# Kernel tuning notes

Measured on AMD Instinct MI355X. Metric: run time of the kernel, lower is better.

Reference implementation:

```python
import jax, jax.numpy as jnp
import numpy as np

BATCH = 32768
NJETS = 10
NCOMBOS = 22
FF = 200
NSEL = 6
EPS = 1e-5
METRIC = jnp.array([1.0, -1.0, -1.0, -1.0], dtype=jnp.float32)  # (E,px,py,pz) Minkowski


def _cola(v, w_combo):
    # v: [b, n, 4]; w_combo: [c, n] -> [b, n+c, 4] (identity rows + learned combos)
    combos = jnp.einsum('cj,bjv->bcv', w_combo, v)
    return jnp.concatenate([v, combos], axis=1)


def _lola(v, w_e, w_d):
    # v: [b, n, 4] -> [b, n, 5] features: m2, pT, E, w_e.E, w_d.d2
    m2 = jnp.einsum('biv,v,biv->bi', v, METRIC, v)           # invariant mass^2
    pt = jnp.sqrt(v[..., 1] ** 2 + v[..., 2] ** 2)           # transverse momentum
    E = v[..., 0]
    we = jnp.einsum('ij,bj->bi', w_e, E)
    # pairwise Minkowski distances via gram trick (avoids [b,n,n,4] tensor)
    gram = jnp.einsum('biv,v,bjv->bij', v, METRIC, v)        # [b, n, n]
    d2 = m2[:, :, None] + m2[:, None, :] - 2.0 * gram
    wd = jnp.einsum('ij,bij->bi', w_d, d2)
    return jnp.stack([m2, pt, E, we, wd], axis=-1)


def _batchnorm(x, gamma, beta):
    # torch BatchNorm1d in train mode: per-feature batch mean / biased var
    mu = jnp.mean(x, axis=0)
    var = jnp.mean((x - mu) ** 2, axis=0)
    return (x - mu) * jax.lax.rsqrt(var + EPS) * gamma + beta


def _head(v, cola_w, w_e, w_d, bn_g, bn_b, w1, b1, w2, b2):
    x = _cola(v, cola_w)
    f = _lola(x, w_e, w_d).reshape(x.shape[0], -1)  # [b, ntotal*5]
    f = _batchnorm(f, bn_g, bn_b)
    h = jax.nn.relu(f @ w1.T + b1)
    return h @ w2.T + b2


def setup_inputs() -> dict:
    key = jax.random.key(0)
    ks = jax.random.split(key, 20)
    n_isr = NJETS + NCOMBOS   # 32
    n_dec = NSEL + NCOMBOS    # 28
    f_isr, f_dec = n_isr * 5, n_dec * 5
    rn = lambda k, s, sc=0.1: jax.random.normal(k, s, jnp.float32) * sc
    return {
        'vectors': jax.random.normal(ks[0], (BATCH, NJETS, 4), jnp.float32),
        'isr_cola_w': rn(ks[1], (NCOMBOS, NJETS)),
        'isr_we': rn(ks[2], (n_isr, n_isr)),
        'isr_wd': rn(ks[3], (n_isr, n_isr)),
        'isr_bn_g': jnp.ones((f_isr,), jnp.float32),
        'isr_bn_b': jnp.zeros((f_isr,), jnp.float32),
        'isr_w1': rn(ks[4], (FF, f_isr)),
        'isr_b1': jnp.zeros((FF,), jnp.float32),
        'isr_w2': rn(ks[5], (NJETS, FF)),
        'isr_b2': jnp.zeros((NJETS,), jnp.float32),
        'dec_cola_w': rn(ks[6], (NCOMBOS, NSEL)),
        'dec_we': rn(ks[7], (n_dec, n_dec)),
        'dec_wd': rn(ks[8], (n_dec, n_dec)),
        'dec_bn_g': jnp.ones((f_dec,), jnp.float32),
        'dec_bn_b': jnp.zeros((f_dec,), jnp.float32),
        'dec_w1': rn(ks[9], (FF, f_dec)),
        'dec_b1': jnp.zeros((FF,), jnp.float32),
        'dec_w2': rn(ks[10], (11, FF)),
        'dec_b2': jnp.zeros((11,), jnp.float32),
    }


def reference(vectors, isr_cola_w, isr_we, isr_wd, isr_bn_g, isr_bn_b,
              isr_w1, isr_b1, isr_w2, isr_b2,
              dec_cola_w, dec_we, dec_wd, dec_bn_g, dec_bn_b,
              dec_w1, dec_b1, dec_w2, dec_b2):
    out_isr = _head(vectors, isr_cola_w, isr_we, isr_wd, isr_bn_g, isr_bn_b,
                    isr_w1, isr_b1, isr_w2, isr_b2)  # [b, njets]
    # iterative argmin+delete of (njets-6) jets == keep top-6 scores, original order
    scores = jax.lax.stop_gradient(out_isr)  # torch code detaches isrtag
    _, idx = jax.lax.top_k(scores, NSEL)
    idx = jnp.sort(idx, axis=1)  # np.delete preserves original ordering
    selected = jnp.take_along_axis(vectors, idx[:, :, None], axis=1)  # [b, 6, 4]
    out_dec = _head(selected, dec_cola_w, dec_we, dec_wd, dec_bn_g, dec_bn_b,
                    dec_w1, dec_b1, dec_w2, dec_b2)  # [b, 11]
    return jnp.concatenate([out_isr, out_dec], axis=1)  # [b, njets+11]
```

## Files before the change

kernel.cpp:

```cpp
#include <hip/hip_runtime.h>


#define BATCH 32768
#define NJ 10
#define FFDIM 200
#define OUTSTRIDE 21
#define NFEATBLK 4096

typedef float v2f __attribute__((ext_vector_type(2)));

template<int NIN, int NP>
__global__ __launch_bounds__(256) void feat_kernel(
    const float* __restrict__ vin,
    const float* __restrict__ cola,
    const float* __restrict__ we,
    const float* __restrict__ wd,
    float* __restrict__ fout,
    float* __restrict__ psum,
    float* __restrict__ psq)
{
    constexpr int NC = 22;
    constexpr int F  = NP * 5;
    constexpr int RB = 8;
    constexpr int SW = NP + 1;
    constexpr int SF = F + 8;
    __shared__ float s_cola[NC * NIN];
    __shared__ float s_we[NP * SW];
    __shared__ float s_wd[NP * SW];
    __shared__ float4 s_x[RB][NP];
    __shared__ float s_m2[RB][NP];
    __shared__ float s_f[RB * SF];

    const int tid = threadIdx.x;
    const int blk = blockIdx.x;

    for (int k = tid; k < NC * NIN; k += 256) s_cola[k] = cola[k];
    for (int k = tid; k < NP * NP; k += 256) {
        const int i2 = k / NP, j2 = k - i2 * NP;
        s_we[i2 * SW + j2] = we[k];
        s_wd[i2 * SW + j2] = wd[k];
    }
    for (int k = tid; k < RB * NIN * 4; k += 256)
        ((float*)&s_x[0][0])[(k / (NIN * 4)) * NP * 4 + (k % (NIN * 4))] =
            vin[(size_t)blk * RB * NIN * 4 + k];
    __syncthreads();

    const int r = tid >> 5;
    const int i = tid & 31;

    if (i >= NIN && i < NP) {
        const int c = i - NIN;
        float4 x = make_float4(0.f, 0.f, 0.f, 0.f);
        #pragma unroll
        for (int j = 0; j < NIN; j++) {
            const float w = s_cola[c * NIN + j];
            const float4 xj = s_x[r][j];
            x.x += w * xj.x; x.y += w * xj.y; x.z += w * xj.z; x.w += w * xj.w;
        }
        s_x[r][i] = x;
    }
    __syncthreads();

    float m2 = 0.f, pt = 0.f;
    float4 xi = make_float4(0.f, 0.f, 0.f, 0.f);
    if (i < NP) {
        xi = s_x[r][i];
        m2 = xi.x * xi.x - xi.y * xi.y - xi.z * xi.z - xi.w * xi.w;
        pt = sqrtf(xi.y * xi.y + xi.z * xi.z);
        s_m2[r][i] = m2;
    }
    __syncthreads();
    if (i < NP) {
        float wesum = 0.f, wdsum = 0.f;
        for (int j = 0; j < NP; j++) {
            const float4 xj = s_x[r][j];
            wesum += s_we[i * SW + j] * xj.x;
            const float g = xi.x * xj.x - xi.y * xj.y - xi.z * xj.z - xi.w * xj.w;
            wdsum += s_wd[i * SW + j] * (m2 + s_m2[r][j] - 2.0f * g);
        }
        s_f[r * SF + i * 5 + 0] = m2;
        s_f[r * SF + i * 5 + 1] = pt;
        s_f[r * SF + i * 5 + 2] = xi.x;
        s_f[r * SF + i * 5 + 3] = wesum;
        s_f[r * SF + i * 5 + 4] = wdsum;
    }
    __syncthreads();

    for (int q = tid; q < RB * F; q += 256) {
        const int rr = q / F, c = q - rr * F;
        fout[(size_t)blk * RB * F + q] = s_f[rr * SF + c];
    }

    if (tid < F) {
        float s = 0.f, s2 = 0.f;
        #pragma unroll
        for (int rr = 0; rr < RB; rr++) {
            const float v = s_f[rr * SF + tid];
            s += v; s2 += v * v;
        }
        psum[(size_t)tid * NFEATBLK + blk] = s;
        psq [(size_t)tid * NFEATBLK + blk] = s2;
    }
}

template<int F>
__global__ __launch_bounds__(256) void bn_reduce(
    const float* __restrict__ psum, const float* __restrict__ psq,
    const float* __restrict__ gamma, const float* __restrict__ beta,
    float* __restrict__ bn)
{
    __shared__ float s1[256], s2[256];
    const int f = blockIdx.x, tid = threadIdx.x;
    float a = 0.f, b = 0.f;
    for (int bk = tid; bk < NFEATBLK; bk += 256) {
        a += psum[(size_t)f * NFEATBLK + bk];
        b += psq [(size_t)f * NFEATBLK + bk];
    }
    s1[tid] = a; s2[tid] = b; __syncthreads();
    for (int s = 128; s > 0; s >>= 1) {
        if (tid < s) { s1[tid] += s1[tid + s]; s2[tid] += s2[tid + s]; }
        __syncthreads();
    }
    if (tid == 0) {
        const float mu  = s1[0] / (float)BATCH;
        const float var = s2[0] / (float)BATCH - mu * mu;
        const float sc  = gamma[f] * rsqrtf(var + 1e-5f);
        bn[f]     = sc;
        bn[F + f] = beta[f] - mu * sc;
    }
}

template<int NF, int NOUT, bool SELECT>
__global__ __launch_bounds__(256, 2) void mlp_kernel(
    const float* __restrict__ fin,
    const float* __restrict__ bn,
    const float* __restrict__ w1,
    const float* __restrict__ b1,
    const float* __restrict__ w2,
    const float* __restrict__ b2,
    const float* __restrict__ vectors,
    float* __restrict__ selout,
    float* __restrict__ out,
    int out_off)
{
    constexpr int RB  = 64;
    constexpr int SU  = 160;
    constexpr int SH  = 228;
    constexpr int SO  = 13;
    constexpr int NCH = NF / 4;
    __shared__ __align__(16) float UH[RB * SH];
    __shared__ __align__(16) float s_w[2][224 * 4];
    __shared__ float s_out[RB * SO];
    __shared__ int   s_idx[RB * 6];

    const int tid = threadIdx.x;
    const int blk = blockIdx.x;
    float* s_scale = &UH[RB * SU];
    float* s_shift = s_scale + NF;

    const int wrow = (tid < 200) ? tid : 199;
    float4 wv;
    if (tid < 224) wv = *reinterpret_cast<const float4*>(w1 + (size_t)wrow * NF);
    for (int k = tid; k < NF; k += 256) { s_scale[k] = bn[k]; s_shift[k] = bn[NF + k]; }
    __syncthreads();

    {
        constexpr int NF4 = NF / 4;
        const float4* fb4 = reinterpret_cast<const float4*>(fin + (size_t)blk * RB * NF);
        for (int q4 = tid; q4 < RB * NF4; q4 += 256) {
            const int row = q4 / NF4, c = (q4 - row * NF4) * 4;
            const float4 v = fb4[q4];
            float4 o;
            o.x = v.x * s_scale[c + 0] + s_shift[c + 0];
            o.y = v.y * s_scale[c + 1] + s_shift[c + 1];
            o.z = v.z * s_scale[c + 2] + s_shift[c + 2];
            o.w = v.w * s_scale[c + 3] + s_shift[c + 3];
            *reinterpret_cast<float4*>(&UH[row * SU + (c ^ ((row >> 3) * 4))]) = o;
        }
    }
    if (tid < 224) {
        *reinterpret_cast<float4*>(&s_w[0][tid * 4]) = wv;
        wv = *reinterpret_cast<const float4*>(w1 + (size_t)wrow * NF + 4);
    }
    __syncthreads();

    const int rg = tid & 7;
    const int ng = tid >> 3;
    v2f acc[7][8];
    #pragma unroll
    for (int j = 0; j < 7; j++)
        #pragma unroll
        for (int i = 0; i < 8; i++) acc[j][i] = (v2f){0.f, 0.f};

    for (int kt = 0; kt < NCH; kt++) {
        const int b = kt & 1;
        const int k4 = kt * 4;
        float4 wq[7], fq[8];
        #pragma unroll
        for (int j = 0; j < 7; j++)
            wq[j] = *reinterpret_cast<const float4*>(&s_w[b][(ng * 7 + j) * 4]);
        #pragma unroll
        for (int i = 0; i < 8; i++)
            fq[i] = *reinterpret_cast<const float4*>(
                &UH[(rg * 8 + i) * SU + (k4 ^ (rg * 4))]);
        #pragma unroll
        for (int j = 0; j < 7; j++) {
            const v2f wlo = (v2f){wq[j].x, wq[j].y};
            const v2f whi = (v2f){wq[j].z, wq[j].w};
            #pragma unroll
            for (int i = 0; i < 8; i++) {
                acc[j][i] += wlo * (v2f){fq[i].x, fq[i].y};
                acc[j][i] += whi * (v2f){fq[i].z, fq[i].w};
            }
        }
        if (tid < 224 && kt + 1 < NCH) {
            *reinterpret_cast<float4*>(&s_w[b ^ 1][tid * 4]) = wv;
            const int kn = (kt + 2 < NCH) ? (kt + 2) * 4 : (NCH - 1) * 4;
            wv = *reinterpret_cast<const float4*>(w1 + (size_t)wrow * NF + kn);
        }
        __syncthreads();
    }

    #pragma unroll
    for (int j = 0; j < 7; j++) {
        const int n = ng * 7 + j;
        if (n < 200) {
            const float bb = b1[n];
            const int n4 = n & ~3, nl = n & 3;
            #pragma unroll
            for (int i = 0; i < 8; i++) {
                const float h = acc[j][i][0] + acc[j][i][1] + bb;
                UH[(rg * 8 + i) * SH + ((n4 ^ (rg * 4)) | nl)] = h > 0.f ? h : 0.f;
            }
        }
    }
    __syncthreads();

    const int w = __builtin_amdgcn_readfirstlane(tid >> 6);
    const int r = tid & 63;
    {
        const int rx = (r >> 3) * 4;
        v2f a2[3];
        #pragma unroll
        for (int m = 0; m < 3; m++) a2[m] = (v2f){0.f, 0.f};
        for (int kc = 0; kc < FFDIM / 4; kc++) {
            const float4 hv = *reinterpret_cast<const float4*>(
                &UH[r * SH + ((kc * 4) ^ rx)]);
            const v2f hlo = (v2f){hv.x, hv.y}, hhi = (v2f){hv.z, hv.w};
            #pragma unroll
            for (int m = 0; m < 3; m++) {
                const int o = w + 4 * m;
                if (o < NOUT) {
                    const float4 w2v = *reinterpret_cast<const float4*>(
                        w2 + (size_t)o * FFDIM + kc * 4);
                    a2[m] += (v2f){w2v.x, w2v.y} * hlo;
                    a2[m] += (v2f){w2v.z, w2v.w} * hhi;
                }
            }
        }
        #pragma unroll
        for (int m = 0; m < 3; m++) {
            const int o = w + 4 * m;
            if (o < NOUT) s_out[r * SO + o] = a2[m][0] + a2[m][1] + b2[o];
        }
    }
    __syncthreads();

    if (SELECT) {
        if (tid < RB) {
            float sc[10];
            #pragma unroll
            for (int o = 0; o < 10; o++) sc[o] = s_out[tid * SO + o];
            bool used[10];
            #pragma unroll
            for (int o = 0; o < 10; o++) used[o] = false;
            int ids[6];
            for (int k = 0; k < 6; k++) {
                float m = -3.0e38f; int mi = 0;
                for (int o = 0; o < 10; o++)
                    if (!used[o] && sc[o] > m) { m = sc[o]; mi = o; }
                used[mi] = true; ids[k] = mi;
            }
            for (int a2i = 1; a2i < 6; a2i++) {
                const int v = ids[a2i]; int bp = a2i - 1;
                while (bp >= 0 && ids[bp] > v) { ids[bp + 1] = ids[bp]; bp--; }
                ids[bp + 1] = v;
            }
            #pragma unroll
            for (int k = 0; k < 6; k++) s_idx[tid * 6 + k] = ids[k];
        }
        __syncthreads();
        for (int q = tid; q < RB * 6; q += 256) {
            const int r2 = q / 6, j = q - r2 * 6;
            reinterpret_cast<float4*>(selout)[(size_t)blk * RB * 6 + q] =
                reinterpret_cast<const float4*>(vectors)
                    [(size_t)(blk * RB + r2) * NJ + s_idx[r2 * 6 + j]];
        }
    }

    for (int q = tid; q < RB * NOUT; q += 256) {
        const int r2 = q / NOUT, o = q - r2 * NOUT;
        out[(size_t)(blk * RB + r2) * OUTSTRIDE + out_off + o] = s_out[r2 * SO + o];
    }
}

extern "C" void kernel_launch(void* const* d_in, const int* in_sizes, int n_in,
                              void* d_out, int out_size, void* d_ws, size_t ws_size,
                              hipStream_t stream) {
    const float* vectors  = (const float*)d_in[0];
    const float* isr_cola = (const float*)d_in[1];
    const float* isr_we   = (const float*)d_in[2];
    const float* isr_wd   = (const float*)d_in[3];
    const float* isr_bn_g = (const float*)d_in[4];
    const float* isr_bn_b = (const float*)d_in[5];
    const float* isr_w1   = (const float*)d_in[6];
    const float* isr_b1   = (const float*)d_in[7];
    const float* isr_w2   = (const float*)d_in[8];
    const float* isr_b2   = (const float*)d_in[9];
    const float* dec_cola = (const float*)d_in[10];
    const float* dec_we   = (const float*)d_in[11];
    const float* dec_wd   = (const float*)d_in[12];
    const float* dec_bn_g = (const float*)d_in[13];
    const float* dec_bn_b = (const float*)d_in[14];
    const float* dec_w1   = (const float*)d_in[15];
    const float* dec_b1   = (const float*)d_in[16];
    const float* dec_w2   = (const float*)d_in[17];
    const float* dec_b2   = (const float*)d_in[18];
    float* out = (float*)d_out;
    float* ws  = (float*)d_ws;

    float* f_buf  = ws;
    float* sel    = f_buf + 5242880;
    float* ps     = sel + 786432;
    float* pq     = ps + 655360;
    float* bn_i   = pq + 655360;
    float* bn_d   = bn_i + 320;

    feat_kernel<10, 32><<<4096, 256, 0, stream>>>(vectors, isr_cola, isr_we, isr_wd,
                                                  f_buf, ps, pq);
    bn_reduce<160><<<160, 256, 0, stream>>>(ps, pq, isr_bn_g, isr_bn_b, bn_i);
    mlp_kernel<160, 10, true><<<512, 256, 0, stream>>>(f_buf, bn_i, isr_w1, isr_b1,
                                                       isr_w2, isr_b2, vectors, sel,
                                                       out, 0);
    feat_kernel<6, 28><<<4096, 256, 0, stream>>>(sel, dec_cola, dec_we, dec_wd,
                                                 f_buf, ps, pq);
    bn_reduce<140><<<140, 256, 0, stream>>>(ps, pq, dec_bn_g, dec_bn_b, bn_d);
    mlp_kernel<140, 11, false><<<512, 256, 0, stream>>>(f_buf, bn_d, dec_w1, dec_b1,
                                                        dec_w2, dec_b2, nullptr, nullptr,
                                                        out, 10);
}
```

Before: 151.0 us.

## Stage W1 tiles per wavefront to drop block barriers in MLP K loop

```diff
diff --git a/kernel.cpp b/kernel.cpp
--- a/kernel.cpp
+++ b/kernel.cpp
@@ -149,18 +149,21 @@
     constexpr int SO  = 13;
     constexpr int NCH = NF / 4;
     __shared__ __align__(16) float UH[RB * SH];
-    __shared__ __align__(16) float s_w[2][224 * 4];
+    __shared__ __align__(16) float s_wv[4][2][56 * 4];
     __shared__ float s_out[RB * SO];
     __shared__ int   s_idx[RB * 6];
 
-    const int tid = threadIdx.x;
-    const int blk = blockIdx.x;
+    const int tid  = threadIdx.x;
+    const int blk  = blockIdx.x;
+    const int lane = tid & 63;
+    const int wvid = __builtin_amdgcn_readfirstlane(tid >> 6);
     float* s_scale = &UH[RB * SU];
     float* s_shift = s_scale + NF;
 
-    const int wrow = (tid < 200) ? tid : 199;
-    float4 wv;
-    if (tid < 224) wv = *reinterpret_cast<const float4*>(w1 + (size_t)wrow * NF);
+    const int nrow  = wvid * 56 + ((lane < 56) ? lane : 55);
+    const int wrowg = (nrow < 200) ? nrow : 199;
+    const float* w1g = w1 + (size_t)wrowg * NF;
+
     for (int k = tid; k < NF; k += 256) { s_scale[k] = bn[k]; s_shift[k] = bn[NF + k]; }
     __syncthreads();
 
@@ -178,27 +181,35 @@
             *reinterpret_cast<float4*>(&UH[row * SU + (c ^ ((row >> 3) * 4))]) = o;
         }
     }
-    if (tid < 224) {
-        *reinterpret_cast<float4*>(&s_w[0][tid * 4]) = wv;
-        wv = *reinterpret_cast<const float4*>(w1 + (size_t)wrow * NF + 4);
-    }
-    __syncthreads();
-
-    const int rg = tid & 7;
-    const int ng = tid >> 3;
+    __syncthreads();
+
+    const int rg  = tid & 7;
+    const int ngl = lane >> 3;
     v2f acc[7][8];
     #pragma unroll
     for (int j = 0; j < 7; j++)
         #pragma unroll
         for (int i = 0; i < 8; i++) acc[j][i] = (v2f){0.f, 0.f};
 
+    {
+        const float4 w0 = *reinterpret_cast<const float4*>(w1g);
+        if (lane < 56) *reinterpret_cast<float4*>(&s_wv[wvid][0][lane * 4]) = w0;
+    }
+    float4 wR = *reinterpret_cast<const float4*>(w1g + ((NCH > 1) ? 4 : 0));
+
     for (int kt = 0; kt < NCH; kt++) {
         const int b = kt & 1;
         const int k4 = kt * 4;
+        if (kt + 1 < NCH && lane < 56)
+            *reinterpret_cast<float4*>(&s_wv[wvid][b ^ 1][lane * 4]) = wR;
+        float4 wN = wR;
+        if (kt + 2 < NCH)
+            wN = *reinterpret_cast<const float4*>(w1g + (kt + 2) * 4);
+
         float4 wq[7], fq[8];
         #pragma unroll
         for (int j = 0; j < 7; j++)
-            wq[j] = *reinterpret_cast<const float4*>(&s_w[b][(ng * 7 + j) * 4]);
+            wq[j] = *reinterpret_cast<const float4*>(&s_wv[wvid][b][(ngl * 7 + j) * 4]);
         #pragma unroll
         for (int i = 0; i < 8; i++)
             fq[i] = *reinterpret_cast<const float4*>(
@@ -213,14 +224,11 @@
                 acc[j][i] += whi * (v2f){fq[i].z, fq[i].w};
             }
         }
-        if (tid < 224 && kt + 1 < NCH) {
-            *reinterpret_cast<float4*>(&s_w[b ^ 1][tid * 4]) = wv;
-            const int kn = (kt + 2 < NCH) ? (kt + 2) * 4 : (NCH - 1) * 4;
-            wv = *reinterpret_cast<const float4*>(w1 + (size_t)wrow * NF + kn);
-        }
-        __syncthreads();
-    }
-
+        wR = wN;
+    }
+    __syncthreads();
+
+    const int ng = tid >> 3;
     #pragma unroll
     for (int j = 0; j < 7; j++) {
         const int n = ng * 7 + j;
@@ -236,8 +244,7 @@
     }
     __syncthreads();
 
-    const int w = __builtin_amdgcn_readfirstlane(tid >> 6);
-    const int r = tid & 63;
+    const int r = lane;
     {
         const int rx = (r >> 3) * 4;
         v2f a2[3];
@@ -249,7 +256,7 @@
             const v2f hlo = (v2f){hv.x, hv.y}, hhi = (v2f){hv.z, hv.w};
             #pragma unroll
             for (int m = 0; m < 3; m++) {
-                const int o = w + 4 * m;
+                const int o = wvid + 4 * m;
                 if (o < NOUT) {
                     const float4 w2v = *reinterpret_cast<const float4*>(
                         w2 + (size_t)o * FFDIM + kc * 4);
@@ -260,7 +267,7 @@
         }
         #pragma unroll
         for (int m = 0; m < 3; m++) {
-            const int o = w + 4 * m;
+            const int o = wvid + 4 * m;
             if (o < NOUT) s_out[r * SO + o] = a2[m][0] + a2[m][1] + b2[o];
         }
     }
```

Measured after the change: 148.6 us. Within noise of the previous version (-1.6%).
